# Performance work log

Measured on AMD Instinct MI355X. Metric: run time of the kernel, lower is better.

## Reference

```python
import jax, jax.numpy as jnp
import numpy as np

B, T, D = 2, 2048, 1024
H, DK, DV, NH = 8, 128, 256, 2  # heads, key dim, value dim (expand_v=2), num_householder
CONV = 4
INTER = 2816
EPS = 1e-6


def rmsnorm(x, w):
    return x * jax.lax.rsqrt(jnp.mean(x * x, -1, keepdims=True) + EPS) * w


def l2norm(x):
    return x * jax.lax.rsqrt(jnp.sum(x * x, -1, keepdims=True) + 1e-6)


def causal_conv_silu(x, w):
    # depthwise causal conv1d with silu activation; x: [B,T,C], w: [C,K]
    K = w.shape[1]
    xp = jnp.pad(x, ((0, 0), (K - 1, 0), (0, 0)))
    y = sum(xp[:, i:i + x.shape[1], :] * w[:, i] for i in range(K))
    return jax.nn.silu(y)


def setup_inputs():
    key = jax.random.key(0)
    ks = jax.random.split(key, 16)
    s = 0.02
    return {
        "hidden_states": jax.random.normal(ks[0], (B, T, D), jnp.float32),
        "attn_norm_w": jnp.ones((D,), jnp.float32),
        "Wq": jax.random.normal(ks[1], (D, H * DK), jnp.float32) * s,
        "Wk": jax.random.normal(ks[2], (D, NH * H * DK), jnp.float32) * s,
        "Wv": jax.random.normal(ks[3], (D, NH * H * DV), jnp.float32) * s,
        "Wb": jax.random.normal(ks[4], (D, H * NH), jnp.float32) * s,
        "Wa": jax.random.normal(ks[5], (D, H), jnp.float32) * s,
        "A_log": jnp.log(jax.random.uniform(ks[6], (H,), jnp.float32, 1.0, 16.0)),
        "dt_bias": jax.random.normal(ks[7], (H,), jnp.float32) * 0.5,
        "conv_q_w": jax.random.normal(ks[8], (H * DK, CONV), jnp.float32) * 0.5,
        "conv_k_w": jax.random.normal(ks[9], (NH * H * DK, CONV), jnp.float32) * 0.5,
        "conv_v_w": jax.random.normal(ks[10], (NH * H * DV, CONV), jnp.float32) * 0.5,
        "Wg": jax.random.normal(ks[11], (D, H * DV), jnp.float32) * s,
        "o_norm_w": jnp.ones((DV,), jnp.float32),
        "Wo": jax.random.normal(ks[12], (H * DV, D), jnp.float32) * s,
        "mlp_norm_w": jnp.ones((D,), jnp.float32),
        "Wgate": jax.random.normal(ks[13], (D, 2 * INTER), jnp.float32) * s,
        "Wdown": jax.random.normal(ks[14], (INTER, D), jnp.float32) * s,
    }


def reference(hidden_states, attn_norm_w, Wq, Wk, Wv, Wb, Wa, A_log, dt_bias,
              conv_q_w, conv_k_w, conv_v_w, Wg, o_norm_w, Wo,
              mlp_norm_w, Wgate, Wdown):
    residual = hidden_states
    x = rmsnorm(hidden_states, attn_norm_w)

    # projections + short conv + silu, then L2-normalized q/k (gated delta rule)
    q = l2norm(causal_conv_silu(x @ Wq, conv_q_w).reshape(B, T, H, DK))
    k = l2norm(causal_conv_silu(x @ Wk, conv_k_w).reshape(B, T, NH, H, DK))
    v = causal_conv_silu(x @ Wv, conv_v_w).reshape(B, T, NH, H, DV)
    beta = jax.nn.sigmoid(x @ Wb).reshape(B, T, H, NH)
    g = -jnp.exp(A_log) * jax.nn.softplus(x @ Wa + dt_bias)  # [B,T,H] log-decay

    def step(S, inp):
        q_t, k_t, v_t, b_t, g_t = inp
        # forget gate applied once per token, then NH Householder delta-rule updates
        S = S * jnp.exp(g_t)[..., None, None]  # S: [B,H,DK,DV]
        for j in range(NH):
            kj, vj, bj = k_t[:, j], v_t[:, j], b_t[..., j]
            kS = jnp.einsum('bhk,bhkv->bhv', kj, S)
            S = S + bj[..., None, None] * jnp.einsum('bhk,bhv->bhkv', kj, vj - kS)
        o_t = jnp.einsum('bhk,bhkv->bhv', q_t, S)
        return S, o_t

    S0 = jnp.zeros((B, H, DK, DV), x.dtype)
    xs = (jnp.swapaxes(q, 0, 1), jnp.swapaxes(k, 0, 1), jnp.swapaxes(v, 0, 1),
          jnp.swapaxes(beta, 0, 1), jnp.swapaxes(g, 0, 1))
    _, o = jax.lax.scan(step, S0, xs)  # [T,B,H,DV]
    o = jnp.swapaxes(o, 0, 1)

    # gated RMSNorm output gate + output projection
    gate = (x @ Wg).reshape(B, T, H, DV)
    o = rmsnorm(o, o_norm_w) * jax.nn.silu(gate)
    hidden = residual + o.reshape(B, T, H * DV) @ Wo

    # GatedMLP (swiglu)
    y = rmsnorm(hidden, mlp_norm_w)
    gate_m, up = jnp.split(y @ Wgate, 2, -1)
    return hidden + (jax.nn.silu(gate_m) * up) @ Wdown
```

## Files before the change

### kernel.cpp

```cpp
#include <hip/hip_runtime.h>
#include <hip/hip_bf16.h>
#include <math.h>

#define Bq 2
#define Tq 2048
#define Dq 1024
#define Hq 8
#define DKq 128
#define DVq 256
#define NHq 2
#define BTq (Bq*Tq)
#define INTERq 2816

typedef __hip_bfloat16 bf16;
typedef short bfv8 __attribute__((ext_vector_type(8)));
typedef float f32v4 __attribute__((ext_vector_type(4)));

__device__ __forceinline__ float b2f(bf16 v){ return __bfloat162float(v); }
__device__ __forceinline__ bf16 f2b(float v){ return __float2bfloat16(v); }
__device__ __forceinline__ float bs2f(short s){
  union { short s; bf16 b; } u; u.s = s; return __bfloat162float(u.b);
}

__device__ __forceinline__ int is_f32(const unsigned* magic){ return magic[0] == 0x3F800000u; }

__device__ __forceinline__ float ldin(const void* p, int f32, size_t i){
  return f32 ? ((const float*)p)[i] : b2f(((const bf16*)p)[i]);
}

__device__ __forceinline__ void gload_lds16(const bf16* g, bf16* lds_uniform){
  __builtin_amdgcn_global_load_lds(
      (const __attribute__((address_space(1))) void*)g,
      (__attribute__((address_space(3))) void*)lds_uniform, 16, 0, 0);
}

__device__ __forceinline__ float wave_sum(float v){
  #pragma unroll
  for (int off = 32; off > 0; off >>= 1) v += __shfl_xor(v, off, 64);
  return v;
}

__device__ __forceinline__ float block_reduce_sum(float v, float* red){
  #pragma unroll
  for (int off = 32; off > 0; off >>= 1) v += __shfl_down(v, off, 64);
  int lane = threadIdx.x & 63, wid = threadIdx.x >> 6;
  if (lane == 0) red[wid] = v;
  __syncthreads();
  int nw = (blockDim.x + 63) >> 6;
  float tot = 0.f;
  for (int i = 0; i < nw; i++) tot += red[i];
  return tot;
}

__global__ __launch_bounds__(256) void rmsnorm_kernel(const void* __restrict__ in, int in_mode,
    const void* __restrict__ w, const unsigned* __restrict__ magic,
    bf16* __restrict__ out){
  __shared__ float red[4];
  int f32 = is_f32(magic);
  int inf32 = in_mode ? 1 : f32;
  size_t row = blockIdx.x;
  int i0 = threadIdx.x * 4;
  float xv[4];
  if (inf32){
    float4 v = *(const float4*)((const float*)in + row*Dq + i0);
    xv[0]=v.x; xv[1]=v.y; xv[2]=v.z; xv[3]=v.w;
  } else {
    short4 s = *(const short4*)((const bf16*)in + row*Dq + i0);
    xv[0]=bs2f(s.x); xv[1]=bs2f(s.y); xv[2]=bs2f(s.z); xv[3]=bs2f(s.w);
  }
  float ss = fmaf(xv[0],xv[0], fmaf(xv[1],xv[1], fmaf(xv[2],xv[2], xv[3]*xv[3])));
  float tot = block_reduce_sum(ss, red);
  float sc = rsqrtf(tot / (float)Dq + 1e-6f);
  bf16 ob[4];
  #pragma unroll
  for (int j = 0; j < 4; j++) ob[j] = f2b(xv[j] * sc * ldin(w, f32, i0 + j));
  *(short4*)(out + row*Dq + i0) = *(short4*)ob;
}

__global__ __launch_bounds__(256) void wsplit_kernel(
    const void* __restrict__ W, const unsigned* __restrict__ magic,
    bf16* __restrict__ hi, bf16* __restrict__ lo, int K, int N){
  __shared__ float tile[32][33];
  int f32 = is_f32(magic);
  int n0 = blockIdx.x * 32, k0 = blockIdx.y * 32;
  int tx = threadIdx.x & 31, ty = threadIdx.x >> 5;
  #pragma unroll
  for (int r = 0; r < 4; r++){
    int kr = ty + r*8;
    tile[kr][tx] = ldin(W, f32, (size_t)(k0 + kr)*N + n0 + tx);
  }
  __syncthreads();
  #pragma unroll
  for (int r = 0; r < 4; r++){
    int nr = ty + r*8;
    float v = tile[tx][nr];
    bf16 h = f2b(v);
    size_t idx = (size_t)(n0 + nr)*K + k0 + tx;
    hi[idx] = h;
    if (f32) lo[idx] = f2b(v - b2f(h));
  }
}

__global__ __launch_bounds__(256) void gemm_mfma_kernel(
    const bf16* __restrict__ A, const bf16* __restrict__ WThi, const bf16* __restrict__ WTlo,
    const unsigned* __restrict__ magic,
    const void* __restrict__ res, int res_mode,
    void* __restrict__ out, int out_mode,
    int M, int N, int K){
  __shared__ bf16 As[2][128*32];
  __shared__ bf16 Bs[2][128*32];
  int f32 = is_f32(magic);
  int tid = threadIdx.x;
  int lane = tid & 63, w = tid >> 6;
  int wm = w >> 1, wn = w & 1;
  int l15 = lane & 15, quad = lane >> 4;
  size_t bm = (size_t)blockIdx.x * 128, bn = (size_t)blockIdx.y * 128;

  f32v4 acc[4][4];
  #pragma unroll
  for (int mt = 0; mt < 4; mt++)
    #pragma unroll
    for (int nt = 0; nt < 4; nt++) acc[mt][nt] = 0.f;

  if (f32){
    const bf16* Ab = A    + (bm + wm*64 + l15)*(size_t)K + quad*8;
    const bf16* Bh = WThi + (bn + wn*64 + l15)*(size_t)K + quad*8;
    const bf16* Bl = WTlo + (bn + wn*64 + l15)*(size_t)K + quad*8;
    for (int k0 = 0; k0 < K; k0 += 32){
      bfv8 a[4];
      #pragma unroll
      for (int mt = 0; mt < 4; mt++)
        a[mt] = *(const bfv8*)(Ab + (size_t)mt*16*K + k0);
      #pragma unroll
      for (int nt = 0; nt < 4; nt++){
        bfv8 bh = *(const bfv8*)(Bh + (size_t)nt*16*K + k0);
        bfv8 bl = *(const bfv8*)(Bl + (size_t)nt*16*K + k0);
        #pragma unroll
        for (int mt = 0; mt < 4; mt++){
          acc[mt][nt] = __builtin_amdgcn_mfma_f32_16x16x32_bf16(a[mt], bh, acc[mt][nt], 0, 0, 0);
          acc[mt][nt] = __builtin_amdgcn_mfma_f32_16x16x32_bf16(a[mt], bl, acc[mt][nt], 0, 0, 0);
        }
      }
    }
  } else {
    int srow = tid >> 2;
    int scol = (tid & 3) * 8;
    const bf16* Ag = A    + (bm + srow)*(size_t)K + scol;
    const bf16* Bg = WThi + (bn + srow)*(size_t)K + scol;
    int wslot = w * 512;
    int nt = K >> 5;

#define STAGE(buf, k0) { \
    const bf16* a0 = Ag + (k0); \
    const bf16* b0 = Bg + (k0); \
    gload_lds16(a0,                 &As[buf][wslot]); \
    gload_lds16(a0 + 64*(size_t)K,  &As[buf][2048 + wslot]); \
    gload_lds16(b0,                 &Bs[buf][wslot]); \
    gload_lds16(b0 + 64*(size_t)K,  &Bs[buf][2048 + wslot]); }

    int aoff = (wm*64 + l15)*32 + quad*8;
    int boff = (wn*64 + l15)*32 + quad*8;

    STAGE(0, 0)
    asm volatile("s_waitcnt vmcnt(0)" ::: "memory");
    __syncthreads();
    for (int t = 0; t < nt; ++t){
      int cur = t & 1;
      if (t + 1 < nt) STAGE(cur ^ 1, (t+1) << 5)
      bfv8 a[4], bb[4];
      #pragma unroll
      for (int mt = 0; mt < 4; mt++)
        a[mt] = *(const bfv8*)(&As[cur][aoff + mt*16*32]);
      #pragma unroll
      for (int nn = 0; nn < 4; nn++)
        bb[nn] = *(const bfv8*)(&Bs[cur][boff + nn*16*32]);
      #pragma unroll
      for (int nn = 0; nn < 4; nn++)
        #pragma unroll
        for (int mt = 0; mt < 4; mt++)
          acc[mt][nn] = __builtin_amdgcn_mfma_f32_16x16x32_bf16(a[mt], bb[nn], acc[mt][nn], 0, 0, 0);
      asm volatile("s_waitcnt vmcnt(0)" ::: "memory");
      __syncthreads();
    }
#undef STAGE
  }

  #pragma unroll
  for (int mt = 0; mt < 4; mt++)
    #pragma unroll
    for (int nt = 0; nt < 4; nt++)
      #pragma unroll
      for (int r = 0; r < 4; r++){
        size_t row = bm + wm*64 + mt*16 + quad*4 + r;
        size_t col = bn + wn*64 + nt*16 + l15;
        float v = acc[mt][nt][r];
        if (res_mode == 1) v += ldin(res, f32, row*N + col);
        else if (res_mode == 2) v += ((const float*)res)[row*N + col];
        if (out_mode == 0) ((float*)out)[row*N + col] = v;
        else if (out_mode == 1) ((bf16*)out)[row*N + col] = f2b(v);
        else { if (f32) ((float*)out)[row*N + col] = v; else ((bf16*)out)[row*N + col] = f2b(v); }
      }
}

__global__ __launch_bounds__(256) void betag_kernel(
    const bf16* __restrict__ x, const void* __restrict__ Wb, const void* __restrict__ Wa,
    const void* __restrict__ A_log, const void* __restrict__ dt_bias,
    const unsigned* __restrict__ magic,
    float* __restrict__ beta, float* __restrict__ eg){
  __shared__ float xs[Dq];
  int f32 = is_f32(magic);
  size_t bt = blockIdx.x;
  for (int i = threadIdx.x; i < Dq; i += 256) xs[i] = b2f(x[bt*Dq + i]);
  __syncthreads();
  int wv = threadIdx.x >> 6, lane = threadIdx.x & 63;
  #pragma unroll
  for (int r = 0; r < 6; r++){
    int n = wv*6 + r;
    float a = 0.f;
    if (n < 16){
      #pragma unroll
      for (int e = 0; e < 16; e++){
        int i = lane + 64*e;
        a = fmaf(xs[i], ldin(Wb, f32, (size_t)i*16 + n), a);
      }
    } else {
      int h = n - 16;
      #pragma unroll
      for (int e = 0; e < 16; e++){
        int i = lane + 64*e;
        a = fmaf(xs[i], ldin(Wa, f32, (size_t)i*8 + h), a);
      }
    }
    #pragma unroll
    for (int off = 32; off > 0; off >>= 1) a += __shfl_down(a, off, 64);
    if (lane == 0){
      if (n < 16){
        int h = n >> 1, j = n & 1;
        beta[(bt*Hq + h)*NHq + j] = 1.f / (1.f + expf(-a));
      } else {
        int h = n - 16;
        a += ldin(dt_bias, f32, h);
        float sp = (a > 20.f) ? a : log1pf(expf(a));
        eg[bt*Hq + h] = expf(-expf(ldin(A_log, f32, h)) * sp);
      }
    }
  }
}

__global__ __launch_bounds__(64) void conv_silu_kernel(
    const bf16* __restrict__ in, const void* __restrict__ w,
    const unsigned* __restrict__ magic,
    float* __restrict__ out, int C){
  int f32 = is_f32(magic);
  int bt = blockIdx.x;
  int t = bt & (Tq - 1);
  int c = blockIdx.y * 128 + threadIdx.x * 2;
  float a0 = 0.f, a1 = 0.f;
  #pragma unroll
  for (int i = 0; i < 4; i++){
    int tt = t - 3 + i;
    if (tt >= 0){
      short2 s = *(const short2*)(in + (size_t)(bt - 3 + i)*C + c);
      a0 = fmaf(bs2f(s.x), ldin(w, f32, (size_t)c*4 + i), a0);
      a1 = fmaf(bs2f(s.y), ldin(w, f32, (size_t)(c+1)*4 + i), a1);
    }
  }
  float y0 = a0 / (1.f + __expf(-a0));
  float y1 = a1 / (1.f + __expf(-a1));
  float tot = wave_sum(fmaf(y0, y0, y1*y1));
  float sc = rsqrtf(tot + 1e-6f);
  *(float2*)(out + (size_t)bt*C + c) = make_float2(y0*sc, y1*sc);
}

__global__ __launch_bounds__(256) void conv_v_kernel(
    const bf16* __restrict__ in, const void* __restrict__ w,
    const unsigned* __restrict__ magic, bf16* __restrict__ out){
  int f32 = is_f32(magic);
  int bt = blockIdx.x;
  int t = bt & (Tq - 1);
  int c = blockIdx.y * 2048 + threadIdx.x * 8;
  float wv[32];
  #pragma unroll
  for (int j = 0; j < 8; j++)
    #pragma unroll
    for (int i = 0; i < 4; i++) wv[j*4+i] = ldin(w, f32, (size_t)(c+j)*4 + i);
  float acc[8] = {0,0,0,0,0,0,0,0};
  #pragma unroll
  for (int i = 0; i < 4; i++){
    int tt = t - 3 + i;
    if (tt >= 0){
      bfv8 v = *(const bfv8*)(in + (size_t)(bt - 3 + i)*4096 + c);
      #pragma unroll
      for (int j = 0; j < 8; j++) acc[j] = fmaf(bs2f(v[j]), wv[j*4+i], acc[j]);
    }
  }
  bf16 ob[8];
  #pragma unroll
  for (int j = 0; j < 8; j++) ob[j] = f2b(acc[j] / (1.f + __expf(-acc[j])));
  *(bfv8*)(out + (size_t)bt*4096 + c) = *(bfv8*)ob;
}

#define DPP_ADD(x, ctrl) ((x) + __int_as_float(__builtin_amdgcn_update_dpp( \
    0, __float_as_int(x), (ctrl), 0xF, 0xF, true)))
#define KRED(p) { p = DPP_ADD(p, 0x128); p = DPP_ADD(p, 0x124); \
                  p = DPP_ADD(p, 0x122); p = DPP_ADD(p, 0x121); }

__global__ __launch_bounds__(64, 1) void scan_kernel(
    const float* __restrict__ qn,
    const float* __restrict__ kn,
    const bf16*  __restrict__ vcv,
    const float* __restrict__ beta,
    const float* __restrict__ eg,
    float* __restrict__ o){
  int bh = blockIdx.x;
  int b = bh >> 3, h = bh & 7;
  int lane = threadIdx.x;
  int kg = lane & 15;
  int vloc = lane >> 4;
  int vv = blockIdx.y * 4 + vloc;
  int c0 = (h << 8) + vv;
  int c1 = 2048 + (h << 8) + vv;
  const size_t base = (size_t)b * Tq;
  const float* knh = kn + base*2048 + h*DKq + kg*8;
  const float* qnh = qn + (base*Hq + h)*(size_t)DKq + kg*8;
  const bf16*  vph = vcv + base*4096;
  const float* gh  = eg + base*Hq + h;
  const float2* bph = (const float2*)(beta + (base*Hq + h)*(size_t)NHq);
  float* oh = o + (base*Hq + h)*(size_t)DVq + vv;

  float4 S0 = {0,0,0,0}, S1 = {0,0,0,0};
#define SDOT(Ka, Kb, p) { \
    float e0 = fmaf(Ka.x, S0.x, Ka.y * S0.y); \
    float e1 = fmaf(Ka.z, S0.z, Ka.w * S0.w); \
    float e2 = fmaf(Kb.x, S1.x, Kb.y * S1.y); \
    float e3 = fmaf(Kb.z, S1.z, Kb.w * S1.w); \
    p = (e0 + e1) + (e2 + e3); }
#define SUPD(Ka, Kb, d) { \
    S0.x = fmaf(Ka.x, d, S0.x); S0.y = fmaf(Ka.y, d, S0.y); \
    S0.z = fmaf(Ka.z, d, S0.z); S0.w = fmaf(Ka.w, d, S0.w); \
    S1.x = fmaf(Kb.x, d, S1.x); S1.y = fmaf(Kb.y, d, S1.y); \
    S1.z = fmaf(Kb.z, d, S1.z); S1.w = fmaf(Kb.w, d, S1.w); }

  float4 A0E = *(const float4*)(knh);
  float4 A1E = *(const float4*)(knh + 4);
  float4 B0E = *(const float4*)(knh + 1024);
  float4 B1E = *(const float4*)(knh + 1028);
  float4 Q0E = *(const float4*)(qnh);
  float4 Q1E = *(const float4*)(qnh + 4);
  float4 A0O = *(const float4*)(knh + 2048);
  float4 A1O = *(const float4*)(knh + 2052);
  float4 B0O = *(const float4*)(knh + 3072);
  float4 B1O = *(const float4*)(knh + 3076);
  float4 Q0O = *(const float4*)(qnh + 1024);
  float4 Q1O = *(const float4*)(qnh + 1028);
  float  gE  = gh[0],   gO  = gh[8];
  float2 beE = bph[0],  beO = bph[8];
  float vaE = b2f(vph[c0]),        vbE = b2f(vph[c1]);
  float vaO = b2f(vph[4096 + c0]), vbO = b2f(vph[4096 + c1]);

#define STEP(A0,A1,B0,B1,Q0,Q1, gS, beS, vaS, vbS, t, tp) { \
    float egv = gS; \
    gS = gh[(tp)*8]; \
    S0.x *= egv; S0.y *= egv; S0.z *= egv; S0.w *= egv; \
    S1.x *= egv; S1.y *= egv; S1.z *= egv; S1.w *= egv; \
     \
    { float p; SDOT(A0, A1, p) \
      KRED(p) \
      float delta = beS.x * (vaS - p); \
      SUPD(A0, A1, delta) \
      A0 = *(const float4*)(knh + (tp)*2048); \
      A1 = *(const float4*)(knh + (tp)*2048 + 4); \
      vaS = b2f(vph[(tp)*4096 + c0]); } \
     \
    { float p; SDOT(B0, B1, p) \
      KRED(p) \
      float delta = beS.y * (vbS - p); \
      SUPD(B0, B1, delta) \
      B0 = *(const float4*)(knh + (tp)*2048 + 1024); \
      B1 = *(const float4*)(knh + (tp)*2048 + 1028); \
      vbS = b2f(vph[(tp)*4096 + c1]); } \
    beS = bph[(tp)*8]; \
     \
    { float p; SDOT(Q0, Q1, p) \
      KRED(p) \
      if ((lane & 15) == 0) oh[(t)*2048] = p; \
      Q0 = *(const float4*)(qnh + (tp)*1024); \
      Q1 = *(const float4*)(qnh + (tp)*1024 + 4); } \
    __builtin_amdgcn_sched_barrier(0); }

  for (int t = 0; t < Tq; t += 2){
    STEP(A0E,A1E,B0E,B1E,Q0E,Q1E, gE,beE,vaE,vbE, t,   t+2)
    STEP(A0O,A1O,B0O,B1O,Q0O,Q1O, gO,beO,vaO,vbO, t+1, t+3)
  }
#undef STEP
#undef SDOT
#undef SUPD
}

__global__ __launch_bounds__(64) void gate_o_kernel(
    const float* __restrict__ o, const void* __restrict__ onw,
    const unsigned* __restrict__ magic,
    const bf16* __restrict__ gate, bf16* __restrict__ og){
  int f32 = is_f32(magic);
  size_t bth = blockIdx.x;
  int d0 = threadIdx.x * 4;
  float4 v = *(const float4*)(o + bth*DVq + d0);
  float tot = wave_sum(fmaf(v.x,v.x, fmaf(v.y,v.y, fmaf(v.z,v.z, v.w*v.w))));
  float sc = rsqrtf(tot / (float)DVq + 1e-6f);
  short4 gs = *(const short4*)(gate + bth*DVq + d0);
  float gv[4] = {bs2f(gs.x), bs2f(gs.y), bs2f(gs.z), bs2f(gs.w)};
  float vv[4] = {v.x, v.y, v.z, v.w};
  bf16 ob[4];
  #pragma unroll
  for (int j = 0; j < 4; j++){
    float silu = gv[j] / (1.f + __expf(-gv[j]));
    ob[j] = f2b(vv[j] * sc * ldin(onw, f32, d0 + j) * silu);
  }
  *(short4*)(og + bth*DVq + d0) = *(short4*)ob;
}

__global__ __launch_bounds__(256) void silumul_kernel(
    const bf16* __restrict__ gu, bf16* __restrict__ mid, int n){
  int i = (blockIdx.x * 256 + threadIdx.x) * 8;
  if (i >= n) return;
  int bt = i / INTERq, c = i % INTERq;
  const bf16* gp = gu + (size_t)bt*2*INTERq + c;
  bfv8 g8 = *(const bfv8*)gp;
  bfv8 u8 = *(const bfv8*)(gp + INTERq);
  bf16 ob[8];
  #pragma unroll
  for (int j = 0; j < 8; j++){
    float gm = bs2f(g8[j]);
    float up = bs2f(u8[j]);
    ob[j] = f2b(gm / (1.f + __expf(-gm)) * up);
  }
  *(bfv8*)(mid + i) = *(bfv8*)ob;
}

extern "C" void kernel_launch(void* const* d_in, const int* in_sizes, int n_in,
                              void* d_out, int out_size, void* d_ws, size_t ws_size,
                              hipStream_t stream){
  const void* hs      = d_in[0];
  const unsigned* magic = (const unsigned*)d_in[1];
  const void* attn_nw = d_in[1];
  const void* Wq      = d_in[2];
  const void* Wk      = d_in[3];
  const void* Wv      = d_in[4];
  const void* Wb      = d_in[5];
  const void* Wa      = d_in[6];
  const void* A_log   = d_in[7];
  const void* dt_bias = d_in[8];
  const void* conv_q  = d_in[9];
  const void* conv_k  = d_in[10];
  const void* conv_v  = d_in[11];
  const void* Wg      = d_in[12];
  const void* o_nw    = d_in[13];
  const void* Wo      = d_in[14];
  const void* mlp_nw  = d_in[15];
  const void* Wgate   = d_in[16];
  const void* Wdown   = d_in[17];

  char* ws = (char*)d_ws;
  const size_t MB = (size_t)1 << 20;
  size_t X     = 0;
  size_t QPRE  = 8*MB;
  size_t KPRE  = 16*MB;
  size_t VPRE  = 32*MB;
  size_t GATE  = 64*MB;
  size_t QN    = 80*MB;
  size_t KN    = 96*MB;
  size_t HID   = 128*MB;
  size_t BETA  = 144*MB;
  size_t Gb    = 144*MB + 512*1024;
  size_t VCV    = 0;
  size_t O      = 32*MB;
  size_t OG     = QN;
  size_t Y      = KN;
  size_t GATEUP = 0;
  size_t MID    = 44*MB;
  size_t W0 = 145*MB;
  size_t WTQh = W0 +  0*MB, WTQl = W0 +  2*MB;
  size_t WTKh = W0 +  4*MB, WTKl = W0 +  8*MB;
  size_t WTVh = W0 + 12*MB, WTVl = W0 + 20*MB;
  size_t WTGh = W0 + 28*MB, WTGl = W0 + 32*MB;
  size_t WTOh = W0 + 36*MB, WTOl = W0 + 40*MB;
  size_t WTUh = W0 + 44*MB, WTUl = W0 + 56*MB;
  size_t WTDh = W0 + 68*MB, WTDl = W0 + 74*MB;
  (void)ws_size; (void)in_sizes; (void)n_in; (void)out_size;

  wsplit_kernel<<<dim3(1024/32, 1024/32), 256, 0, stream>>>(Wq,    magic, (bf16*)(ws+WTQh), (bf16*)(ws+WTQl), 1024, 1024);
  wsplit_kernel<<<dim3(2048/32, 1024/32), 256, 0, stream>>>(Wk,    magic, (bf16*)(ws+WTKh), (bf16*)(ws+WTKl), 1024, 2048);
  wsplit_kernel<<<dim3(4096/32, 1024/32), 256, 0, stream>>>(Wv,    magic, (bf16*)(ws+WTVh), (bf16*)(ws+WTVl), 1024, 4096);
  wsplit_kernel<<<dim3(2048/32, 1024/32), 256, 0, stream>>>(Wg,    magic, (bf16*)(ws+WTGh), (bf16*)(ws+WTGl), 1024, 2048);
  wsplit_kernel<<<dim3(1024/32, 2048/32), 256, 0, stream>>>(Wo,    magic, (bf16*)(ws+WTOh), (bf16*)(ws+WTOl), 2048, 1024);
  wsplit_kernel<<<dim3(5632/32, 1024/32), 256, 0, stream>>>(Wgate, magic, (bf16*)(ws+WTUh), (bf16*)(ws+WTUl), 1024, 5632);
  wsplit_kernel<<<dim3(1024/32, 2816/32), 256, 0, stream>>>(Wdown, magic, (bf16*)(ws+WTDh), (bf16*)(ws+WTDl), 2816, 1024);

  rmsnorm_kernel<<<BTq, 256, 0, stream>>>(hs, 0, attn_nw, magic, (bf16*)(ws+X));

  gemm_mfma_kernel<<<dim3(32,  8), 256, 0, stream>>>((bf16*)(ws+X), (bf16*)(ws+WTQh), (bf16*)(ws+WTQl), magic, nullptr, 0, ws+QPRE, 1, BTq, 1024, 1024);
  gemm_mfma_kernel<<<dim3(32, 16), 256, 0, stream>>>((bf16*)(ws+X), (bf16*)(ws+WTKh), (bf16*)(ws+WTKl), magic, nullptr, 0, ws+KPRE, 1, BTq, 2048, 1024);
  gemm_mfma_kernel<<<dim3(32, 32), 256, 0, stream>>>((bf16*)(ws+X), (bf16*)(ws+WTVh), (bf16*)(ws+WTVl), magic, nullptr, 0, ws+VPRE, 1, BTq, 4096, 1024);
  gemm_mfma_kernel<<<dim3(32, 16), 256, 0, stream>>>((bf16*)(ws+X), (bf16*)(ws+WTGh), (bf16*)(ws+WTGl), magic, nullptr, 0, ws+GATE, 1, BTq, 2048, 1024);
  betag_kernel<<<BTq, 256, 0, stream>>>((bf16*)(ws+X), Wb, Wa, A_log, dt_bias, magic, (float*)(ws+BETA), (float*)(ws+Gb));

  conv_silu_kernel<<<dim3(BTq, 1024/128), 64, 0, stream>>>((bf16*)(ws+QPRE), conv_q, magic, (float*)(ws+QN), 1024);
  conv_silu_kernel<<<dim3(BTq, 2048/128), 64, 0, stream>>>((bf16*)(ws+KPRE), conv_k, magic, (float*)(ws+KN), 2048);
  conv_v_kernel<<<dim3(BTq, 2), 256, 0, stream>>>((bf16*)(ws+VPRE), conv_v, magic, (bf16*)(ws+VCV));

  scan_kernel<<<dim3(Bq*Hq, DVq/4), 64, 0, stream>>>(
      (const float*)(ws+QN), (const float*)(ws+KN), (const bf16*)(ws+VCV),
      (const float*)(ws+BETA), (const float*)(ws+Gb), (float*)(ws+O));

  gate_o_kernel<<<BTq*Hq, 64, 0, stream>>>((const float*)(ws+O), o_nw, magic, (const bf16*)(ws+GATE), (bf16*)(ws+OG));

  gemm_mfma_kernel<<<dim3(32, 8), 256, 0, stream>>>((bf16*)(ws+OG), (bf16*)(ws+WTOh), (bf16*)(ws+WTOl), magic, hs, 1, ws+HID, 0, BTq, 1024, 2048);

  rmsnorm_kernel<<<BTq, 256, 0, stream>>>(ws+HID, 1, mlp_nw, magic, (bf16*)(ws+Y));

  gemm_mfma_kernel<<<dim3(32, 44), 256, 0, stream>>>((bf16*)(ws+Y), (bf16*)(ws+WTUh), (bf16*)(ws+WTUl), magic, nullptr, 0, ws+GATEUP, 1, BTq, 5632, 1024);

  int nmid = BTq * INTERq;
  silumul_kernel<<<(nmid/8 + 255)/256, 256, 0, stream>>>((const bf16*)(ws+GATEUP), (bf16*)(ws+MID), nmid);

  gemm_mfma_kernel<<<dim3(32, 8), 256, 0, stream>>>((bf16*)(ws+MID), (bf16*)(ws+WTDh), (bf16*)(ws+WTDl), magic, ws+HID, 2, d_out, 2, BTq, 1024, 2816);
}
```

Before: 2.493 ms.

## Batch weight splits, fuse QKVG GEMMs, rmsnorm+betag, conv q/k, and SwiGLU epilogue

Merges the seven weight-split launches into one kernel and fuses rmsnorm into the beta/gate kernel. It also replaces the four Q/K/V/G GEMM launches with one grouped GEMM and merges the q/k conv kernels. The gate/up weight is written interleaved so the gate+up GEMM can apply SiLU-multiply in its epilogue, which removes the separate silumul pass and the large intermediate buffer. The aim is fewer launches and less memory traffic, at the cost of more complex indexing.

```diff
diff --git a/kernel.cpp b/kernel.cpp
--- a/kernel.cpp
+++ b/kernel.cpp
@@ -52,37 +52,32 @@
   return tot;
 }
 
-__global__ __launch_bounds__(256) void rmsnorm_kernel(const void* __restrict__ in, int in_mode,
-    const void* __restrict__ w, const unsigned* __restrict__ magic,
-    bf16* __restrict__ out){
-  __shared__ float red[4];
-  int f32 = is_f32(magic);
-  int inf32 = in_mode ? 1 : f32;
-  size_t row = blockIdx.x;
-  int i0 = threadIdx.x * 4;
-  float xv[4];
-  if (inf32){
-    float4 v = *(const float4*)((const float*)in + row*Dq + i0);
-    xv[0]=v.x; xv[1]=v.y; xv[2]=v.z; xv[3]=v.w;
-  } else {
-    short4 s = *(const short4*)((const bf16*)in + row*Dq + i0);
-    xv[0]=bs2f(s.x); xv[1]=bs2f(s.y); xv[2]=bs2f(s.z); xv[3]=bs2f(s.w);
-  }
-  float ss = fmaf(xv[0],xv[0], fmaf(xv[1],xv[1], fmaf(xv[2],xv[2], xv[3]*xv[3])));
-  float tot = block_reduce_sum(ss, red);
-  float sc = rsqrtf(tot / (float)Dq + 1e-6f);
-  bf16 ob[4];
-  #pragma unroll
-  for (int j = 0; j < 4; j++) ob[j] = f2b(xv[j] * sc * ldin(w, f32, i0 + j));
-  *(short4*)(out + row*Dq + i0) = *(short4*)ob;
-}
-
-__global__ __launch_bounds__(256) void wsplit_kernel(
-    const void* __restrict__ W, const unsigned* __restrict__ magic,
-    bf16* __restrict__ hi, bf16* __restrict__ lo, int K, int N){
+
+struct WSplitArgs {
+  const void* W[7];
+  bf16* hi[7];
+  bf16* lo[7];
+  int K[7];
+  int N[7];
+  int il[7];
+  int cum[8];
+};
+
+__global__ __launch_bounds__(256) void wsplit_all_kernel(WSplitArgs a,
+    const unsigned* __restrict__ magic){
   __shared__ float tile[32][33];
   int f32 = is_f32(magic);
-  int n0 = blockIdx.x * 32, k0 = blockIdx.y * 32;
+  int bid = blockIdx.x;
+  int wi = 0;
+  #pragma unroll
+  for (int i = 1; i < 7; i++) if (bid >= a.cum[i]) wi = i;
+  int rem = bid - a.cum[wi];
+  const void* W = a.W[wi];
+  bf16* hi = a.hi[wi];
+  bf16* lo = a.lo[wi];
+  int K = a.K[wi], N = a.N[wi], il = a.il[wi];
+  int nbx = N >> 5;
+  int n0 = (rem % nbx) * 32, k0 = (rem / nbx) * 32;
   int tx = threadIdx.x & 31, ty = threadIdx.x >> 5;
   #pragma unroll
   for (int r = 0; r < 4; r++){
@@ -90,14 +85,95 @@
     tile[kr][tx] = ldin(W, f32, (size_t)(k0 + kr)*N + n0 + tx);
   }
   __syncthreads();
+  int NH2 = N >> 1;
   #pragma unroll
   for (int r = 0; r < 4; r++){
-    int nr = ty + r*8;
-    float v = tile[tx][nr];
+    int nl = ty + r*8;
+    int nr = n0 + nl;
+    float v = tile[tx][nl];
     bf16 h = f2b(v);
-    size_t idx = (size_t)(n0 + nr)*K + k0 + tx;
+    int cp = nr;
+    if (il) cp = (nr < NH2) ? (((nr >> 4) << 5) | (nr & 15))
+                            : ((((nr - NH2) >> 4) << 5) | 16 | ((nr - NH2) & 15));
+    size_t idx = (size_t)cp*K + k0 + tx;
     hi[idx] = h;
     if (f32) lo[idx] = f2b(v - b2f(h));
+  }
+}
+
+__device__ __forceinline__ void gemm_acc_bf16(const bf16* __restrict__ A,
+    const bf16* __restrict__ Bh, int K, size_t bm, size_t bn,
+    bf16* As, bf16* Bs, f32v4 (&acc)[4][4]){
+  int tid = threadIdx.x;
+  int lane = tid & 63, w = tid >> 6;
+  int wm = w >> 1, wn = w & 1;
+  int l15 = lane & 15, quad = lane >> 4;
+  int srow = tid >> 2;
+  int scol = (tid & 3) * 8;
+  const bf16* Ag = A  + (bm + srow)*(size_t)K + scol;
+  const bf16* Bg = Bh + (bn + srow)*(size_t)K + scol;
+  int wslot = w * 512;
+  int ntiles = K >> 5;
+  int aoff = (wm*64 + l15)*32 + quad*8;
+  int boff = (wn*64 + l15)*32 + quad*8;
+
+#define STAGE(buf, k0) { \
+    const bf16* a0 = Ag + (k0); \
+    const bf16* b0 = Bg + (k0); \
+    gload_lds16(a0,                &As[(buf)*4096 + wslot]); \
+    gload_lds16(a0 + 64*(size_t)K, &As[(buf)*4096 + 2048 + wslot]); \
+    gload_lds16(b0,                &Bs[(buf)*4096 + wslot]); \
+    gload_lds16(b0 + 64*(size_t)K, &Bs[(buf)*4096 + 2048 + wslot]); }
+
+  STAGE(0, 0)
+  asm volatile("s_waitcnt vmcnt(0)" ::: "memory");
+  __syncthreads();
+  for (int t = 0; t < ntiles; ++t){
+    int cur = t & 1;
+    if (t + 1 < ntiles) STAGE(cur ^ 1, (t+1) << 5)
+    bfv8 a[4], bb[4];
+    #pragma unroll
+    for (int mt = 0; mt < 4; mt++)
+      a[mt] = *(const bfv8*)(&As[cur*4096 + aoff + mt*16*32]);
+    #pragma unroll
+    for (int nn = 0; nn < 4; nn++)
+      bb[nn] = *(const bfv8*)(&Bs[cur*4096 + boff + nn*16*32]);
+    #pragma unroll
+    for (int nn = 0; nn < 4; nn++)
+      #pragma unroll
+      for (int mt = 0; mt < 4; mt++)
+        acc[mt][nn] = __builtin_amdgcn_mfma_f32_16x16x32_bf16(a[mt], bb[nn], acc[mt][nn], 0, 0, 0);
+    asm volatile("s_waitcnt vmcnt(0)" ::: "memory");
+    __syncthreads();
+  }
+#undef STAGE
+}
+
+__device__ __forceinline__ void gemm_acc_f32(const bf16* __restrict__ A,
+    const bf16* __restrict__ Bh0, const bf16* __restrict__ Bl0,
+    int K, size_t bm, size_t bn, f32v4 (&acc)[4][4]){
+  int tid = threadIdx.x;
+  int lane = tid & 63, w = tid >> 6;
+  int wm = w >> 1, wn = w & 1;
+  int l15 = lane & 15, quad = lane >> 4;
+  const bf16* Ab = A   + (bm + wm*64 + l15)*(size_t)K + quad*8;
+  const bf16* Bh = Bh0 + (bn + wn*64 + l15)*(size_t)K + quad*8;
+  const bf16* Bl = Bl0 + (bn + wn*64 + l15)*(size_t)K + quad*8;
+  for (int k0 = 0; k0 < K; k0 += 32){
+    bfv8 a[4];
+    #pragma unroll
+    for (int mt = 0; mt < 4; mt++)
+      a[mt] = *(const bfv8*)(Ab + (size_t)mt*16*K + k0);
+    #pragma unroll
+    for (int nt = 0; nt < 4; nt++){
+      bfv8 bh = *(const bfv8*)(Bh + (size_t)nt*16*K + k0);
+      bfv8 bl = *(const bfv8*)(Bl + (size_t)nt*16*K + k0);
+      #pragma unroll
+      for (int mt = 0; mt < 4; mt++){
+        acc[mt][nt] = __builtin_amdgcn_mfma_f32_16x16x32_bf16(a[mt], bh, acc[mt][nt], 0, 0, 0);
+        acc[mt][nt] = __builtin_amdgcn_mfma_f32_16x16x32_bf16(a[mt], bl, acc[mt][nt], 0, 0, 0);
+      }
+    }
   }
 }
 
@@ -107,8 +183,8 @@
     const void* __restrict__ res, int res_mode,
     void* __restrict__ out, int out_mode,
     int M, int N, int K){
-  __shared__ bf16 As[2][128*32];
-  __shared__ bf16 Bs[2][128*32];
+  __shared__ bf16 As[2*128*32];
+  __shared__ bf16 Bs[2*128*32];
   int f32 = is_f32(magic);
   int tid = threadIdx.x;
   int lane = tid & 63, w = tid >> 6;
@@ -122,69 +198,23 @@
     #pragma unroll
     for (int nt = 0; nt < 4; nt++) acc[mt][nt] = 0.f;
 
-  if (f32){
-    const bf16* Ab = A    + (bm + wm*64 + l15)*(size_t)K + quad*8;
-    const bf16* Bh = WThi + (bn + wn*64 + l15)*(size_t)K + quad*8;
-    const bf16* Bl = WTlo + (bn + wn*64 + l15)*(size_t)K + quad*8;
-    for (int k0 = 0; k0 < K; k0 += 32){
-      bfv8 a[4];
-      #pragma unroll
-      for (int mt = 0; mt < 4; mt++)
-        a[mt] = *(const bfv8*)(Ab + (size_t)mt*16*K + k0);
-      #pragma unroll
-      for (int nt = 0; nt < 4; nt++){
-        bfv8 bh = *(const bfv8*)(Bh + (size_t)nt*16*K + k0);
-        bfv8 bl = *(const bfv8*)(Bl + (size_t)nt*16*K + k0);
+  if (f32) gemm_acc_f32(A, WThi, WTlo, K, bm, bn, acc);
+  else     gemm_acc_bf16(A, WThi, K, bm, bn, As, Bs, acc);
+
+  if (out_mode == 3){
+    #pragma unroll
+    for (int mt = 0; mt < 4; mt++)
+      #pragma unroll
+      for (int nt = 0; nt < 4; nt += 2)
         #pragma unroll
-        for (int mt = 0; mt < 4; mt++){
-          acc[mt][nt] = __builtin_amdgcn_mfma_f32_16x16x32_bf16(a[mt], bh, acc[mt][nt], 0, 0, 0);
-          acc[mt][nt] = __builtin_amdgcn_mfma_f32_16x16x32_bf16(a[mt], bl, acc[mt][nt], 0, 0, 0);
+        for (int r = 0; r < 4; r++){
+          size_t row = bm + wm*64 + mt*16 + quad*4 + r;
+          size_t col = (bn >> 1) + wn*32 + (nt >> 1)*16 + l15;
+          float g = acc[mt][nt][r], u = acc[mt][nt+1][r];
+          ((bf16*)out)[row*INTERq + col] = f2b(g / (1.f + __expf(-g)) * u);
         }
-      }
-    }
-  } else {
-    int srow = tid >> 2;
-    int scol = (tid & 3) * 8;
-    const bf16* Ag = A    + (bm + srow)*(size_t)K + scol;
-    const bf16* Bg = WThi + (bn + srow)*(size_t)K + scol;
-    int wslot = w * 512;
-    int nt = K >> 5;
-
-#define STAGE(buf, k0) { \
-    const bf16* a0 = Ag + (k0); \
-    const bf16* b0 = Bg + (k0); \
-    gload_lds16(a0,                 &As[buf][wslot]); \
-    gload_lds16(a0 + 64*(size_t)K,  &As[buf][2048 + wslot]); \
-    gload_lds16(b0,                 &Bs[buf][wslot]); \
-    gload_lds16(b0 + 64*(size_t)K,  &Bs[buf][2048 + wslot]); }
-
-    int aoff = (wm*64 + l15)*32 + quad*8;
-    int boff = (wn*64 + l15)*32 + quad*8;
-
-    STAGE(0, 0)
-    asm volatile("s_waitcnt vmcnt(0)" ::: "memory");
-    __syncthreads();
-    for (int t = 0; t < nt; ++t){
-      int cur = t & 1;
-      if (t + 1 < nt) STAGE(cur ^ 1, (t+1) << 5)
-      bfv8 a[4], bb[4];
-      #pragma unroll
-      for (int mt = 0; mt < 4; mt++)
-        a[mt] = *(const bfv8*)(&As[cur][aoff + mt*16*32]);
-      #pragma unroll
-      for (int nn = 0; nn < 4; nn++)
-        bb[nn] = *(const bfv8*)(&Bs[cur][boff + nn*16*32]);
-      #pragma unroll
-      for (int nn = 0; nn < 4; nn++)
-        #pragma unroll
-        for (int mt = 0; mt < 4; mt++)
-          acc[mt][nn] = __builtin_amdgcn_mfma_f32_16x16x32_bf16(a[mt], bb[nn], acc[mt][nn], 0, 0, 0);
-      asm volatile("s_waitcnt vmcnt(0)" ::: "memory");
-      __syncthreads();
-    }
-#undef STAGE
-  }
-
+    return;
+  }
   #pragma unroll
   for (int mt = 0; mt < 4; mt++)
     #pragma unroll
@@ -202,16 +232,85 @@
       }
 }
 
-__global__ __launch_bounds__(256) void betag_kernel(
-    const bf16* __restrict__ x, const void* __restrict__ Wb, const void* __restrict__ Wa,
+struct QkvgArgs {
+  const bf16* bh[4];
+  const bf16* bl[4];
+  bf16* out[4];
+  int N[4];
+  int yoff[5];
+};
+
+__global__ __launch_bounds__(256) void gemm_qkvg_kernel(
+    const bf16* __restrict__ A, QkvgArgs a, const unsigned* __restrict__ magic){
+  __shared__ bf16 As[2*128*32];
+  __shared__ bf16 Bs[2*128*32];
+  int f32 = is_f32(magic);
+  int y = blockIdx.y;
+  int g = 0;
+  #pragma unroll
+  for (int i = 1; i < 4; i++) if (y >= a.yoff[i]) g = i;
+  size_t bm = (size_t)blockIdx.x * 128;
+  size_t bn = (size_t)(y - a.yoff[g]) * 128;
+  int N = a.N[g];
+
+  f32v4 acc[4][4];
+  #pragma unroll
+  for (int mt = 0; mt < 4; mt++)
+    #pragma unroll
+    for (int nt = 0; nt < 4; nt++) acc[mt][nt] = 0.f;
+
+  if (f32) gemm_acc_f32(A, a.bh[g], a.bl[g], 1024, bm, bn, acc);
+  else     gemm_acc_bf16(A, a.bh[g], 1024, bm, bn, As, Bs, acc);
+
+  bf16* out = a.out[g];
+  int tid = threadIdx.x;
+  int lane = tid & 63, w = tid >> 6;
+  int wm = w >> 1, wn = w & 1;
+  int l15 = lane & 15, quad = lane >> 4;
+  #pragma unroll
+  for (int mt = 0; mt < 4; mt++)
+    #pragma unroll
+    for (int nt = 0; nt < 4; nt++)
+      #pragma unroll
+      for (int r = 0; r < 4; r++){
+        size_t row = bm + wm*64 + mt*16 + quad*4 + r;
+        size_t col = bn + wn*64 + nt*16 + l15;
+        out[row*N + col] = f2b(acc[mt][nt][r]);
+      }
+}
+
+__global__ __launch_bounds__(256) void rmsnorm_betag_kernel(
+    const void* __restrict__ hs, const void* __restrict__ attn_nw,
+    const void* __restrict__ Wb, const void* __restrict__ Wa,
     const void* __restrict__ A_log, const void* __restrict__ dt_bias,
     const unsigned* __restrict__ magic,
-    float* __restrict__ beta, float* __restrict__ eg){
+    bf16* __restrict__ xout, float* __restrict__ beta, float* __restrict__ eg){
   __shared__ float xs[Dq];
+  __shared__ float red[4];
   int f32 = is_f32(magic);
   size_t bt = blockIdx.x;
-  for (int i = threadIdx.x; i < Dq; i += 256) xs[i] = b2f(x[bt*Dq + i]);
+  int i0 = threadIdx.x * 4;
+  float xv[4];
+  if (f32){
+    float4 v = *(const float4*)((const float*)hs + bt*Dq + i0);
+    xv[0]=v.x; xv[1]=v.y; xv[2]=v.z; xv[3]=v.w;
+  } else {
+    short4 s = *(const short4*)((const bf16*)hs + bt*Dq + i0);
+    xv[0]=bs2f(s.x); xv[1]=bs2f(s.y); xv[2]=bs2f(s.z); xv[3]=bs2f(s.w);
+  }
+  float ss = fmaf(xv[0],xv[0], fmaf(xv[1],xv[1], fmaf(xv[2],xv[2], xv[3]*xv[3])));
+  float tot = block_reduce_sum(ss, red);
+  float sc = rsqrtf(tot / (float)Dq + 1e-6f);
+  bf16 ob[4];
+  #pragma unroll
+  for (int j = 0; j < 4; j++){
+    float xn = xv[j] * sc * ldin(attn_nw, f32, i0 + j);
+    ob[j] = f2b(xn);
+    xs[i0 + j] = xn;
+  }
+  *(short4*)(xout + bt*Dq + i0) = *(short4*)ob;
   __syncthreads();
+
   int wv = threadIdx.x >> 6, lane = threadIdx.x & 63;
   #pragma unroll
   for (int r = 0; r < 6; r++){
@@ -247,14 +346,44 @@
   }
 }
 
-__global__ __launch_bounds__(64) void conv_silu_kernel(
-    const bf16* __restrict__ in, const void* __restrict__ w,
+__global__ __launch_bounds__(256) void rmsnorm_kernel(const void* __restrict__ in, int in_mode,
+    const void* __restrict__ w, const unsigned* __restrict__ magic,
+    bf16* __restrict__ out){
+  __shared__ float red[4];
+  int f32 = is_f32(magic);
+  int inf32 = in_mode ? 1 : f32;
+  size_t row = blockIdx.x;
+  int i0 = threadIdx.x * 4;
+  float xv[4];
+  if (inf32){
+    float4 v = *(const float4*)((const float*)in + row*Dq + i0);
+    xv[0]=v.x; xv[1]=v.y; xv[2]=v.z; xv[3]=v.w;
+  } else {
+    short4 s = *(const short4*)((const bf16*)in + row*Dq + i0);
+    xv[0]=bs2f(s.x); xv[1]=bs2f(s.y); xv[2]=bs2f(s.z); xv[3]=bs2f(s.w);
+  }
+  float ss = fmaf(xv[0],xv[0], fmaf(xv[1],xv[1], fmaf(xv[2],xv[2], xv[3]*xv[3])));
+  float tot = block_reduce_sum(ss, red);
+  float sc = rsqrtf(tot / (float)Dq + 1e-6f);
+  bf16 ob[4];
+  #pragma unroll
+  for (int j = 0; j < 4; j++) ob[j] = f2b(xv[j] * sc * ldin(w, f32, i0 + j));
+  *(short4*)(out + row*Dq + i0) = *(short4*)ob;
+}
+
+__global__ __launch_bounds__(64) void conv_qk_kernel(
+    const bf16* __restrict__ qpre, const bf16* __restrict__ kpre,
+    const void* __restrict__ wq, const void* __restrict__ wk,
     const unsigned* __restrict__ magic,
-    float* __restrict__ out, int C){
+    float* __restrict__ qn, float* __restrict__ kn){
   int f32 = is_f32(magic);
   int bt = blockIdx.x;
   int t = bt & (Tq - 1);
-  int c = blockIdx.y * 128 + threadIdx.x * 2;
+  int yb = blockIdx.y;
+  const bf16* in; const void* w; int C, cb; float* outf;
+  if (yb < 8){ in = qpre; w = wq; C = 1024; cb = yb;     outf = qn; }
+  else       { in = kpre; w = wk; C = 2048; cb = yb - 8; outf = kn; }
+  int c = cb*128 + threadIdx.x*2;
   float a0 = 0.f, a1 = 0.f;
   #pragma unroll
   for (int i = 0; i < 4; i++){
@@ -269,7 +398,7 @@
   float y1 = a1 / (1.f + __expf(-a1));
   float tot = wave_sum(fmaf(y0, y0, y1*y1));
   float sc = rsqrtf(tot + 1e-6f);
-  *(float2*)(out + (size_t)bt*C + c) = make_float2(y0*sc, y1*sc);
+  *(float2*)(outf + (size_t)bt*C + c) = make_float2(y0*sc, y1*sc);
 }
 
 __global__ __launch_bounds__(256) void conv_v_kernel(
@@ -363,7 +492,6 @@
     gS = gh[(tp)*8]; \
     S0.x *= egv; S0.y *= egv; S0.z *= egv; S0.w *= egv; \
     S1.x *= egv; S1.y *= egv; S1.z *= egv; S1.w *= egv; \
-     \
     { float p; SDOT(A0, A1, p) \
       KRED(p) \
       float delta = beS.x * (vaS - p); \
@@ -371,7 +499,6 @@
       A0 = *(const float4*)(knh + (tp)*2048); \
       A1 = *(const float4*)(knh + (tp)*2048 + 4); \
       vaS = b2f(vph[(tp)*4096 + c0]); } \
-     \
     { float p; SDOT(B0, B1, p) \
       KRED(p) \
       float delta = beS.y * (vbS - p); \
@@ -380,7 +507,6 @@
       B1 = *(const float4*)(knh + (tp)*2048 + 1028); \
       vbS = b2f(vph[(tp)*4096 + c1]); } \
     beS = bph[(tp)*8]; \
-     \
     { float p; SDOT(Q0, Q1, p) \
       KRED(p) \
       if ((lane & 15) == 0) oh[(t)*2048] = p; \
@@ -417,24 +543,6 @@
     ob[j] = f2b(vv[j] * sc * ldin(onw, f32, d0 + j) * silu);
   }
   *(short4*)(og + bth*DVq + d0) = *(short4*)ob;
-}
-
-__global__ __launch_bounds__(256) void silumul_kernel(
-    const bf16* __restrict__ gu, bf16* __restrict__ mid, int n){
-  int i = (blockIdx.x * 256 + threadIdx.x) * 8;
-  if (i >= n) return;
-  int bt = i / INTERq, c = i % INTERq;
-  const bf16* gp = gu + (size_t)bt*2*INTERq + c;
-  bfv8 g8 = *(const bfv8*)gp;
-  bfv8 u8 = *(const bfv8*)(gp + INTERq);
-  bf16 ob[8];
-  #pragma unroll
-  for (int j = 0; j < 8; j++){
-    float gm = bs2f(g8[j]);
-    float up = bs2f(u8[j]);
-    ob[j] = f2b(gm / (1.f + __expf(-gm)) * up);
-  }
-  *(bfv8*)(mid + i) = *(bfv8*)ob;
 }
 
 extern "C" void kernel_launch(void* const* d_in, const int* in_sizes, int n_in,
@@ -476,8 +584,7 @@
   size_t O      = 32*MB;
   size_t OG     = QN;
   size_t Y      = KN;
-  size_t GATEUP = 0;
-  size_t MID    = 44*MB;
+  size_t MID    = O;
   size_t W0 = 145*MB;
   size_t WTQh = W0 +  0*MB, WTQl = W0 +  2*MB;
   size_t WTKh = W0 +  4*MB, WTKl = W0 +  8*MB;
@@ -488,40 +595,60 @@
   size_t WTDh = W0 + 68*MB, WTDl = W0 + 74*MB;
   (void)ws_size; (void)in_sizes; (void)n_in; (void)out_size;
 
-  wsplit_kernel<<<dim3(1024/32, 1024/32), 256, 0, stream>>>(Wq,    magic, (bf16*)(ws+WTQh), (bf16*)(ws+WTQl), 1024, 1024);
-  wsplit_kernel<<<dim3(2048/32, 1024/32), 256, 0, stream>>>(Wk,    magic, (bf16*)(ws+WTKh), (bf16*)(ws+WTKl), 1024, 2048);
-  wsplit_kernel<<<dim3(4096/32, 1024/32), 256, 0, stream>>>(Wv,    magic, (bf16*)(ws+WTVh), (bf16*)(ws+WTVl), 1024, 4096);
-  wsplit_kernel<<<dim3(2048/32, 1024/32), 256, 0, stream>>>(Wg,    magic, (bf16*)(ws+WTGh), (bf16*)(ws+WTGl), 1024, 2048);
-  wsplit_kernel<<<dim3(1024/32, 2048/32), 256, 0, stream>>>(Wo,    magic, (bf16*)(ws+WTOh), (bf16*)(ws+WTOl), 2048, 1024);
-  wsplit_kernel<<<dim3(5632/32, 1024/32), 256, 0, stream>>>(Wgate, magic, (bf16*)(ws+WTUh), (bf16*)(ws+WTUl), 1024, 5632);
-  wsplit_kernel<<<dim3(1024/32, 2816/32), 256, 0, stream>>>(Wdown, magic, (bf16*)(ws+WTDh), (bf16*)(ws+WTDl), 2816, 1024);
-
-  rmsnorm_kernel<<<BTq, 256, 0, stream>>>(hs, 0, attn_nw, magic, (bf16*)(ws+X));
-
-  gemm_mfma_kernel<<<dim3(32,  8), 256, 0, stream>>>((bf16*)(ws+X), (bf16*)(ws+WTQh), (bf16*)(ws+WTQl), magic, nullptr, 0, ws+QPRE, 1, BTq, 1024, 1024);
-  gemm_mfma_kernel<<<dim3(32, 16), 256, 0, stream>>>((bf16*)(ws+X), (bf16*)(ws+WTKh), (bf16*)(ws+WTKl), magic, nullptr, 0, ws+KPRE, 1, BTq, 2048, 1024);
-  gemm_mfma_kernel<<<dim3(32, 32), 256, 0, stream>>>((bf16*)(ws+X), (bf16*)(ws+WTVh), (bf16*)(ws+WTVl), magic, nullptr, 0, ws+VPRE, 1, BTq, 4096, 1024);
-  gemm_mfma_kernel<<<dim3(32, 16), 256, 0, stream>>>((bf16*)(ws+X), (bf16*)(ws+WTGh), (bf16*)(ws+WTGl), magic, nullptr, 0, ws+GATE, 1, BTq, 2048, 1024);
-  betag_kernel<<<BTq, 256, 0, stream>>>((bf16*)(ws+X), Wb, Wa, A_log, dt_bias, magic, (float*)(ws+BETA), (float*)(ws+Gb));
-
-  conv_silu_kernel<<<dim3(BTq, 1024/128), 64, 0, stream>>>((bf16*)(ws+QPRE), conv_q, magic, (float*)(ws+QN), 1024);
-  conv_silu_kernel<<<dim3(BTq, 2048/128), 64, 0, stream>>>((bf16*)(ws+KPRE), conv_k, magic, (float*)(ws+KN), 2048);
-  conv_v_kernel<<<dim3(BTq, 2), 256, 0, stream>>>((bf16*)(ws+VPRE), conv_v, magic, (bf16*)(ws+VCV));
+  WSplitArgs wa;
+  {
+    const void* Ws[7]  = {Wq, Wk, Wv, Wg, Wo, Wgate, Wdown};
+    size_t hio[7]      = {WTQh, WTKh, WTVh, WTGh, WTOh, WTUh, WTDh};
+    size_t loo[7]      = {WTQl, WTKl, WTVl, WTGl, WTOl, WTUl, WTDl};
+    int Ks[7]          = {1024, 1024, 1024, 1024, 2048, 1024, 2816};
+    int Ns[7]          = {1024, 2048, 4096, 2048, 1024, 5632, 1024};
+    int ils[7]         = {0, 0, 0, 0, 0, 1, 0};
+    int cums[8]        = {0, 1024, 3072, 7168, 9216, 11264, 16896, 19712};
+    for (int i = 0; i < 7; i++){
+      wa.W[i] = Ws[i]; wa.hi[i] = (bf16*)(ws + hio[i]); wa.lo[i] = (bf16*)(ws + loo[i]);
+      wa.K[i] = Ks[i]; wa.N[i] = Ns[i]; wa.il[i] = ils[i]; wa.cum[i] = cums[i];
+    }
+    wa.cum[7] = cums[7];
+    wsplit_all_kernel<<<19712, 256, 0, stream>>>(wa, magic);
+  }
+
+  rmsnorm_betag_kernel<<<BTq, 256, 0, stream>>>(hs, attn_nw, Wb, Wa, A_log, dt_bias,
+      magic, (bf16*)(ws+X), (float*)(ws+BETA), (float*)(ws+Gb));
+
+  QkvgArgs qa;
+  {
+    size_t bho[4] = {WTQh, WTKh, WTVh, WTGh};
+    size_t blo[4] = {WTQl, WTKl, WTVl, WTGl};
+    size_t oo[4]  = {QPRE, KPRE, VPRE, GATE};
+    int Ns[4]     = {1024, 2048, 4096, 2048};
+    int yo[5]     = {0, 8, 24, 56, 72};
+    for (int i = 0; i < 4; i++){
+      qa.bh[i] = (const bf16*)(ws + bho[i]); qa.bl[i] = (const bf16*)(ws + blo[i]);
+      qa.out[i] = (bf16*)(ws + oo[i]); qa.N[i] = Ns[i]; qa.yoff[i] = yo[i];
+    }
+    qa.yoff[4] = yo[4];
+    gemm_qkvg_kernel<<<dim3(32, 72), 256, 0, stream>>>((const bf16*)(ws+X), qa, magic);
+  }
+
+  conv_qk_kernel<<<dim3(BTq, 24), 64, 0, stream>>>((const bf16*)(ws+QPRE), (const bf16*)(ws+KPRE),
+      conv_q, conv_k, magic, (float*)(ws+QN), (float*)(ws+KN));
+  conv_v_kernel<<<dim3(BTq, 2), 256, 0, stream>>>((const bf16*)(ws+VPRE), conv_v, magic, (bf16*)(ws+VCV));
 
   scan_kernel<<<dim3(Bq*Hq, DVq/4), 64, 0, stream>>>(
       (const float*)(ws+QN), (const float*)(ws+KN), (const bf16*)(ws+VCV),
       (const float*)(ws+BETA), (const float*)(ws+Gb), (float*)(ws+O));
 
-  gate_o_kernel<<<BTq*Hq, 64, 0, stream>>>((const float*)(ws+O), o_nw, magic, (const bf16*)(ws+GATE), (bf16*)(ws+OG));
-
-  gemm_mfma_kernel<<<dim3(32, 8), 256, 0, stream>>>((bf16*)(ws+OG), (bf16*)(ws+WTOh), (bf16*)(ws+WTOl), magic, hs, 1, ws+HID, 0, BTq, 1024, 2048);
+  gate_o_kernel<<<BTq*Hq, 64, 0, stream>>>((const float*)(ws+O), o_nw, magic,
+      (const bf16*)(ws+GATE), (bf16*)(ws+OG));
+
+  gemm_mfma_kernel<<<dim3(32, 8), 256, 0, stream>>>((bf16*)(ws+OG), (bf16*)(ws+WTOh), (bf16*)(ws+WTOl),
+      magic, hs, 1, ws+HID, 0, BTq, 1024, 2048);
 
   rmsnorm_kernel<<<BTq, 256, 0, stream>>>(ws+HID, 1, mlp_nw, magic, (bf16*)(ws+Y));
 
-  gemm_mfma_kernel<<<dim3(32, 44), 256, 0, stream>>>((bf16*)(ws+Y), (bf16*)(ws+WTUh), (bf16*)(ws+WTUl), magic, nullptr, 0, ws+GATEUP, 1, BTq, 5632, 1024);
-
-  int nmid = BTq * INTERq;
-  silumul_kernel<<<(nmid/8 + 255)/256, 256, 0, stream>>>((const bf16*)(ws+GATEUP), (bf16*)(ws+MID), nmid);
-
-  gemm_mfma_kernel<<<dim3(32, 8), 256, 0, stream>>>((bf16*)(ws+MID), (bf16*)(ws+WTDh), (bf16*)(ws+WTDl), magic, ws+HID, 2, d_out, 2, BTq, 1024, 2816);
-}
+  gemm_mfma_kernel<<<dim3(32, 44), 256, 0, stream>>>((bf16*)(ws+Y), (bf16*)(ws+WTUh), (bf16*)(ws+WTUl),
+      magic, nullptr, 0, ws+MID, 3, BTq, 5632, 1024);
+
+  gemm_mfma_kernel<<<dim3(32, 8), 256, 0, stream>>>((bf16*)(ws+MID), (bf16*)(ws+WTDh), (bf16*)(ws+WTDl),
+      magic, ws+HID, 2, d_out, 2, BTq, 1024, 2816);
+}
```

After: 2.352 ms. 1.06x faster.
